# Optimization experiments

Hardware: AMD Instinct MI355X
Metric: run time of the kernel (lower is better)

The kernel has to match this reference:

```python
import jax, jax.numpy as jnp
import numpy as np

B, S, H = 32, 512, 2048
FP, SP = 1024, 1024


def setup_inputs() -> dict:
    key = jax.random.key(0)
    ks = jax.random.split(key, 8)
    X = jax.random.normal(ks[0], (B, S, H), dtype=jnp.float32)
    pY = jax.random.randint(ks[1], (B, S), 0, 3)
    # Y must be consistent with pY: hcw rows index [2, 2+FP), roo rows [2+FP, 2+FP+SP)
    y_hcw = jax.random.randint(ks[2], (B, S), 2, 2 + FP)
    y_roo = jax.random.randint(ks[3], (B, S), 2 + FP, 2 + FP + SP)
    Y = jnp.where(pY == 1, y_hcw, jnp.where(pY == 2, y_roo, 0))
    sc = 1.0 / np.sqrt(H)
    W_end = jax.random.normal(ks[4], (1, H), dtype=jnp.float32) * sc
    b_end = jnp.zeros((1,), jnp.float32)
    W_hcw = jax.random.normal(ks[5], (FP, H), dtype=jnp.float32) * sc
    b_hcw = jnp.zeros((FP,), jnp.float32)
    W_roo = jax.random.normal(ks[6], (SP, H), dtype=jnp.float32) * sc
    b_roo = jnp.zeros((SP,), jnp.float32)
    return {"X": X, "pY": pY, "Y": Y, "W_end": W_end, "b_end": b_end,
            "W_hcw": W_hcw, "b_hcw": b_hcw, "W_roo": W_roo, "b_roo": b_roo}


def reference(X, pY, Y, W_end, b_end, W_hcw, b_hcw, W_roo, b_roo):
    b, s, h = X.shape
    N = b * s
    Xf = X.reshape(N, h)
    pYf = pY.reshape(N)
    Yf = Y.reshape(N)

    end_mask = pYf == 0
    hcw_mask = pYf == 1
    roo_mask = pYf == 2

    # end head (Bernoulli prob)
    end_logit = Xf @ W_end.T + b_end            # [N, 1]
    end_prob = jax.nn.sigmoid(end_logit)[:, 0]  # [N]
    non_end = 1.0 - end_prob

    # hcw / roo heads: dense compute over all tokens, masked results match
    # the torch gather/scatter exactly at valid positions.
    P_hcw = jax.nn.softmax(Xf @ W_hcw.T + b_hcw, axis=-1)  # [N, FP]
    P_roo = jax.nn.softmax(Xf @ W_roo.T + b_roo, axis=-1)  # [N, SP]

    fp = W_hcw.shape[0]
    sp = W_roo.shape[0]
    idx_hcw = jnp.clip(Yf - 2, 0, fp - 1)
    idx_roo = jnp.clip(Yf - 2 - fp, 0, sp - 1)
    prob_hcw = jnp.take_along_axis(P_hcw, idx_hcw[:, None], axis=1)[:, 0]
    prob_roo = jnp.take_along_axis(P_roo, idx_roo[:, None], axis=1)[:, 0]

    prob = jnp.where(end_mask, end_prob,
                     jnp.where(hcw_mask, prob_hcw * non_end,
                               jnp.where(roo_mask, prob_roo * non_end, 1.0)))

    em = end_mask.astype(X.dtype)[:, None]
    hm = hcw_mask.astype(X.dtype)[:, None]
    rm = roo_mask.astype(X.dtype)[:, None]
    col_end = jnp.broadcast_to(end_prob[:, None], (N, 2)) * em        # [N, 2]
    col_hcw = P_hcw * non_end[:, None] * hm                           # [N, FP]
    col_roo = P_roo * non_end[:, None] * rm                           # [N, SP]
    prob_all_mat = jnp.concatenate([col_end, col_hcw, col_roo], axis=-1)

    log_prob = jnp.log(prob)
    return log_prob.reshape(b, s), prob_all_mat.reshape(b, s, fp + sp + 2)
```

## Files before the change

kernel.cpp:

```cpp
#include <hip/hip_runtime.h>
#include <hip/hip_bf16.h>
#include <cstddef>
#include <cstdint>

#define N_TOK 16384
#define H_    2048
#define FP_   1024
#define SP_   1024
#define C_    2050

#define BM 128
#define BN 128
#define BK 64
#define KP 72

typedef short bf16x8 __attribute__((ext_vector_type(8)));
typedef float f32x4  __attribute__((ext_vector_type(4)));

__device__ __forceinline__ unsigned pack_bf2(float a, float b) {
  __hip_bfloat16 x = __float2bfloat16(a);
  __hip_bfloat16 y = __float2bfloat16(b);
  unsigned short ux, uy;
  __builtin_memcpy(&ux, &x, 2);
  __builtin_memcpy(&uy, &y, 2);
  return (unsigned)ux | ((unsigned)uy << 16);
}

__device__ __forceinline__ unsigned short f2bf(float f) {
  __hip_bfloat16 h = __float2bfloat16(f);
  unsigned short u;
  __builtin_memcpy(&u, &h, 2);
  return u;
}

__device__ __forceinline__ float bf2f(unsigned short u) {
  unsigned v = (unsigned)u << 16;
  float f;
  __builtin_memcpy(&f, &v, 4);
  return f;
}

__global__ __launch_bounds__(256) void convert_kernel(
    const float* __restrict__ X,
    const float* __restrict__ W_hcw, const float* __restrict__ W_roo,
    const float* __restrict__ W_end, const float* __restrict__ b_end,
    unsigned short* __restrict__ Xb, unsigned short* __restrict__ Wb,
    float* __restrict__ mat)
{
  const int wave = threadIdx.x >> 6;
  const int lane = threadIdx.x & 63;
  const int row  = (blockIdx.x << 2) + wave;
  const bool isX = row < N_TOK;
  const float* src;
  unsigned short* dst;
  if (isX) {
    src = X + (size_t)row * H_;
    dst = Xb + (size_t)row * H_;
  } else {
    const int m = row - N_TOK;
    src = (m < FP_) ? (W_hcw + (size_t)m * H_) : (W_roo + (size_t)(m - FP_) * H_);
    dst = Wb + (size_t)m * H_;
  }
  float s = 0.f;
#pragma unroll
  for (int i = 0; i < 8; ++i) {
    const int e = (lane << 2) + (i << 8);
    float4 v = *(const float4*)(src + e);
    uint2 p;
    p.x = pack_bf2(v.x, v.y);
    p.y = pack_bf2(v.z, v.w);
    *(uint2*)(dst + e) = p;
    if (isX) {
      float4 w = *(const float4*)(W_end + e);
      s += v.x * w.x + v.y * w.y + v.z * w.z + v.w * w.w;
    }
  }
  if (isX) {
#pragma unroll
    for (int o = 32; o; o >>= 1) s += __shfl_xor(s, o);
    if (lane == 0) mat[(size_t)row * C_] = s + b_end[0];
  }
}

__global__ __launch_bounds__(512) void gemm_8phase_kernel(
    const unsigned short* __restrict__ Xb, const unsigned short* __restrict__ Wb,
    const float* __restrict__ b_hcw, const float* __restrict__ b_roo,
    float* __restrict__ mat)
{
  __shared__ __align__(16) unsigned short As[2][256 * 64];
  __shared__ __align__(16) unsigned short Bs[2][256 * 64];

  const int c0 = blockIdx.x * 256;
  const int n0 = blockIdx.y * 256;
  const float* bias = (c0 < FP_) ? (b_hcw + c0) : (b_roo + (c0 - FP_));

  const int t    = threadIdx.x;
  const int wave = t >> 6;
  const int lane = t & 63;
  const int wr   = wave >> 2;
  const int wc   = wave & 3;
  const int quad = lane >> 4;
  const int l16  = lane & 15;
  const int sw   = l16 & 7;

  const int srow = t >> 3;
  const int gch  = (t & 7) ^ (srow & 7);
  const unsigned short* gA = Xb + (size_t)(n0 + srow) * H_ + (gch << 3);
  const unsigned short* gB = Wb + (size_t)(c0 + srow) * H_ + (gch << 3);
  const int lds_off = srow * 64 + ((t & 7) << 3);

  auto stage = [&](int buf, int k0) {
#pragma unroll
    for (int r = 0; r < 4; ++r) {
      __builtin_amdgcn_global_load_lds(
          (const __attribute__((address_space(1))) unsigned int*)(gA + (size_t)(r * 64) * H_ + k0),
          (__attribute__((address_space(3))) unsigned int*)(&As[buf][r * 4096 + lds_off]),
          16, 0, 0);
      __builtin_amdgcn_global_load_lds(
          (const __attribute__((address_space(1))) unsigned int*)(gB + (size_t)(r * 64) * H_ + k0),
          (__attribute__((address_space(3))) unsigned int*)(&Bs[buf][r * 4096 + lds_off]),
          16, 0, 0);
    }
  };

  f32x4 acc[8][4];
#pragma unroll
  for (int i = 0; i < 8; ++i)
#pragma unroll
    for (int j = 0; j < 4; ++j)
#pragma unroll
      for (int r = 0; r < 4; ++r) acc[i][j][r] = 0.f;

  const int arow = wr * 128 + l16;
  const int brow = wc * 64 + l16;

  stage(0, 0);
  stage(1, 64);

  bf16x8 a[4][2], b[2][2];

#pragma unroll 1
  for (int tk = 0; tk < 32; ++tk) {
    const int cur = tk & 1;
    if (tk < 31) { asm volatile("s_waitcnt vmcnt(8)" ::: "memory"); }
    else         { asm volatile("s_waitcnt vmcnt(0)" ::: "memory"); }
    __builtin_amdgcn_sched_barrier(0);
    __builtin_amdgcn_s_barrier();

    const unsigned short* A_ = &As[cur][0];
    const unsigned short* B_ = &Bs[cur][0];

#pragma unroll
    for (int i = 0; i < 4; ++i)
#pragma unroll
      for (int kk = 0; kk < 2; ++kk)
        a[i][kk] = *(const bf16x8*)&A_[(arow + i * 16) * 64 + ((((kk << 2) + quad) ^ sw) << 3)];
#pragma unroll
    for (int j = 0; j < 2; ++j)
#pragma unroll
      for (int kk = 0; kk < 2; ++kk)
        b[j][kk] = *(const bf16x8*)&B_[(brow + j * 16) * 64 + ((((kk << 2) + quad) ^ sw) << 3)];
    __builtin_amdgcn_s_barrier();
    asm volatile("s_waitcnt lgkmcnt(0)" ::: "memory");
    __builtin_amdgcn_sched_barrier(0);
    __builtin_amdgcn_s_setprio(1);
#pragma unroll
    for (int i = 0; i < 4; ++i)
#pragma unroll
      for (int j = 0; j < 2; ++j)
#pragma unroll
        for (int kk = 0; kk < 2; ++kk)
          acc[i][j] = __builtin_amdgcn_mfma_f32_16x16x32_bf16(a[i][kk], b[j][kk], acc[i][j], 0, 0, 0);
    __builtin_amdgcn_s_setprio(0);
    __builtin_amdgcn_s_barrier();

#pragma unroll
    for (int j = 0; j < 2; ++j)
#pragma unroll
      for (int kk = 0; kk < 2; ++kk)
        b[j][kk] = *(const bf16x8*)&B_[(brow + (j + 2) * 16) * 64 + ((((kk << 2) + quad) ^ sw) << 3)];
    __builtin_amdgcn_s_barrier();
    asm volatile("s_waitcnt lgkmcnt(0)" ::: "memory");
    __builtin_amdgcn_sched_barrier(0);
    __builtin_amdgcn_s_setprio(1);
#pragma unroll
    for (int i = 0; i < 4; ++i)
#pragma unroll
      for (int j = 0; j < 2; ++j)
#pragma unroll
        for (int kk = 0; kk < 2; ++kk)
          acc[i][j + 2] = __builtin_amdgcn_mfma_f32_16x16x32_bf16(a[i][kk], b[j][kk], acc[i][j + 2], 0, 0, 0);
    __builtin_amdgcn_s_setprio(0);
    __builtin_amdgcn_s_barrier();

#pragma unroll
    for (int i = 0; i < 4; ++i)
#pragma unroll
      for (int kk = 0; kk < 2; ++kk)
        a[i][kk] = *(const bf16x8*)&A_[(arow + (i + 4) * 16) * 64 + ((((kk << 2) + quad) ^ sw) << 3)];
    __builtin_amdgcn_s_barrier();
    asm volatile("s_waitcnt lgkmcnt(0)" ::: "memory");
    __builtin_amdgcn_sched_barrier(0);
    __builtin_amdgcn_s_setprio(1);
#pragma unroll
    for (int i = 0; i < 4; ++i)
#pragma unroll
      for (int j = 0; j < 2; ++j)
#pragma unroll
        for (int kk = 0; kk < 2; ++kk)
          acc[i + 4][j + 2] = __builtin_amdgcn_mfma_f32_16x16x32_bf16(a[i][kk], b[j][kk], acc[i + 4][j + 2], 0, 0, 0);
    __builtin_amdgcn_s_setprio(0);
    __builtin_amdgcn_s_barrier();

#pragma unroll
    for (int j = 0; j < 2; ++j)
#pragma unroll
      for (int kk = 0; kk < 2; ++kk)
        b[j][kk] = *(const bf16x8*)&B_[(brow + j * 16) * 64 + ((((kk << 2) + quad) ^ sw) << 3)];
    __builtin_amdgcn_s_barrier();
    asm volatile("s_waitcnt lgkmcnt(0)" ::: "memory");
    __builtin_amdgcn_sched_barrier(0);
    __builtin_amdgcn_s_setprio(1);
#pragma unroll
    for (int i = 0; i < 4; ++i)
#pragma unroll
      for (int j = 0; j < 2; ++j)
#pragma unroll
        for (int kk = 0; kk < 2; ++kk)
          acc[i + 4][j] = __builtin_amdgcn_mfma_f32_16x16x32_bf16(a[i][kk], b[j][kk], acc[i + 4][j], 0, 0, 0);
    __builtin_amdgcn_s_setprio(0);
    __builtin_amdgcn_s_barrier();

    if (tk < 30) stage(cur, (tk + 2) << 6);
  }

  float bj[4];
#pragma unroll
  for (int j = 0; j < 4; ++j) bj[j] = bias[wc * 64 + j * 16 + l16];
#pragma unroll
  for (int i = 0; i < 8; ++i) {
#pragma unroll
    for (int r = 0; r < 4; ++r) {
      const int row = n0 + wr * 128 + i * 16 + quad * 4 + r;
      unsigned short* dst =
          (unsigned short*)(mat + (size_t)row * C_ + 4) + c0 + wc * 64 + l16;
#pragma unroll
      for (int j = 0; j < 4; ++j) dst[j * 16] = f2bf(acc[i][j][r] + bj[j]);
    }
  }
}

__global__ __launch_bounds__(256) void end_head_kernel(
    const float* __restrict__ X, const float* __restrict__ W_end,
    const float* __restrict__ b_end, float* __restrict__ mat)
{
  const int wave = threadIdx.x >> 6;
  const int lane = threadIdx.x & 63;
  const int n = (blockIdx.x << 2) + wave;
  const float* x = X + (size_t)n * H_;
  float s = 0.f;
#pragma unroll
  for (int i = 0; i < 8; ++i) {
    const int e = (lane + (i << 6)) << 2;
    float4 xv = *(const float4*)(x + e);
    float4 wv = *(const float4*)(W_end + e);
    s += xv.x * wv.x + xv.y * wv.y + xv.z * wv.z + xv.w * wv.w;
  }
#pragma unroll
  for (int o = 32; o; o >>= 1) s += __shfl_xor(s, o);
  if (lane == 0) mat[(size_t)n * C_] = s + b_end[0];
}

__global__ __launch_bounds__(256) void logits_gemm_fused(
    const float* __restrict__ X,
    const float* __restrict__ W_hcw, const float* __restrict__ W_roo,
    const float* __restrict__ b_hcw, const float* __restrict__ b_roo,
    float* __restrict__ mat)
{
  __shared__ __align__(16) unsigned short As[BM * KP];
  __shared__ __align__(16) unsigned short Bs[BN * KP];

  const int c0 = blockIdx.x * BN;
  const int n0 = blockIdx.y * BM;
  const float* Wbase = (c0 < FP_) ? (W_hcw + (size_t)c0 * H_)
                                  : (W_roo + (size_t)(c0 - FP_) * H_);
  const float* bias  = (c0 < FP_) ? (b_hcw + c0) : (b_roo + (c0 - FP_));

  const int t    = threadIdx.x;
  const int wave = t >> 6;
  const int lane = t & 63;
  const int wy   = wave >> 1;
  const int wx   = wave & 1;
  const int quad = lane >> 4;
  const int l16  = lane & 15;
  const int tq = t & 3;
  const int tr = t >> 2;

  f32x4 acc[4][4];
#pragma unroll
  for (int i = 0; i < 4; ++i)
#pragma unroll
    for (int j = 0; j < 4; ++j)
#pragma unroll
      for (int r = 0; r < 4; ++r) acc[i][j][r] = 0.f;

  for (int k0 = 0; k0 < H_; k0 += BK) {
#pragma unroll
    for (int p = 0; p < 2; ++p) {
      const int row = tr + (p << 6);
      const float4* xs = (const float4*)(X + (size_t)(n0 + row) * H_ + k0 + (tq << 4));
      const float4* ws = (const float4*)(Wbase + (size_t)row * H_ + k0 + (tq << 4));
      float4 x0 = xs[0], x1 = xs[1], x2 = xs[2], x3 = xs[3];
      float4 w0 = ws[0], w1 = ws[1], w2 = ws[2], w3 = ws[3];
      uint4 ua0 = {pack_bf2(x0.x, x0.y), pack_bf2(x0.z, x0.w),
                   pack_bf2(x1.x, x1.y), pack_bf2(x1.z, x1.w)};
      uint4 ua1 = {pack_bf2(x2.x, x2.y), pack_bf2(x2.z, x2.w),
                   pack_bf2(x3.x, x3.y), pack_bf2(x3.z, x3.w)};
      uint4 ub0 = {pack_bf2(w0.x, w0.y), pack_bf2(w0.z, w0.w),
                   pack_bf2(w1.x, w1.y), pack_bf2(w1.z, w1.w)};
      uint4 ub1 = {pack_bf2(w2.x, w2.y), pack_bf2(w2.z, w2.w),
                   pack_bf2(w3.x, w3.y), pack_bf2(w3.z, w3.w)};
      *(uint4*)&As[row * KP + (tq << 4)]     = ua0;
      *(uint4*)&As[row * KP + (tq << 4) + 8] = ua1;
      *(uint4*)&Bs[row * KP + (tq << 4)]     = ub0;
      *(uint4*)&Bs[row * KP + (tq << 4) + 8] = ub1;
    }
    __syncthreads();
#pragma unroll
    for (int kk = 0; kk < 2; ++kk) {
      bf16x8 af[4], bfr[4];
#pragma unroll
      for (int i = 0; i < 4; ++i)
        af[i] = *(const bf16x8*)&As[(wy * 64 + i * 16 + l16) * KP + kk * 32 + quad * 8];
#pragma unroll
      for (int j = 0; j < 4; ++j)
        bfr[j] = *(const bf16x8*)&Bs[(wx * 64 + j * 16 + l16) * KP + kk * 32 + quad * 8];
#pragma unroll
      for (int i = 0; i < 4; ++i)
#pragma unroll
        for (int j = 0; j < 4; ++j)
          acc[i][j] = __builtin_amdgcn_mfma_f32_16x16x32_bf16(af[i], bfr[j], acc[i][j], 0, 0, 0);
    }
    __syncthreads();
  }

  float bj[4];
#pragma unroll
  for (int j = 0; j < 4; ++j) bj[j] = bias[wx * 64 + j * 16 + l16];
#pragma unroll
  for (int i = 0; i < 4; ++i) {
#pragma unroll
    for (int r = 0; r < 4; ++r) {
      const int row = n0 + wy * 64 + i * 16 + quad * 4 + r;
      unsigned short* dst =
          (unsigned short*)(mat + (size_t)row * C_ + 4) + c0 + wx * 64 + l16;
#pragma unroll
      for (int j = 0; j < 4; ++j) dst[j * 16] = f2bf(acc[i][j][r] + bj[j]);
    }
  }
}

__global__ __launch_bounds__(256) void epilogue_kernel(
    const int* __restrict__ pY, const int* __restrict__ Yf,
    float* __restrict__ logp, float* __restrict__ mat)
{
  __shared__ float red[4];
  const int n = blockIdx.x;
  const int t = threadIdx.x;
  float* row = mat + (size_t)n * C_;
  const unsigned short* lg = (const unsigned short*)(row + 4);

  const int py = pY[n];
  const int y  = Yf[n];

  uint2 p0 = *(const uint2*)(lg + (t << 3));
  uint2 p1 = *(const uint2*)(lg + (t << 3) + 4);
  const float z = row[0];
  const int ih = min(max(y - 2, 0), FP_ - 1);
  const int ir = min(max(y - 2 - FP_, 0), SP_ - 1);
  const float lh = bf2f(lg[ih]);
  const float lr = bf2f(lg[FP_ + ir]);

  unsigned u[4] = {p0.x, p0.y, p1.x, p1.y};
  float e8[8];
  float s = 0.f;
#pragma unroll
  for (int i = 0; i < 4; ++i) {
    e8[2 * i]     = expf(bf2f((unsigned short)(u[i] & 0xffffu)));
    e8[2 * i + 1] = expf(bf2f((unsigned short)(u[i] >> 16)));
    s += e8[2 * i] + e8[2 * i + 1];
  }
#pragma unroll
  for (int o = 32; o; o >>= 1) s += __shfl_xor(s, o);
  const int w = t >> 6;
  if ((t & 63) == 0) red[w] = s;
  __syncthreads();
  const float Sh = red[0] + red[1];
  const float Sr = red[2] + red[3];

  const float sig = 1.f / (1.f + expf(-z));
  const float ne  = 1.f - sig;
  const float sc = (t < 128) ? ((py == 1) ? ne / Sh : 0.f)
                             : ((py == 2) ? ne / Sr : 0.f);
  float2* wp = (float2*)(row + 2 + (t << 3));
  wp[0] = make_float2(e8[0] * sc, e8[1] * sc);
  wp[1] = make_float2(e8[2] * sc, e8[3] * sc);
  wp[2] = make_float2(e8[4] * sc, e8[5] * sc);
  wp[3] = make_float2(e8[6] * sc, e8[7] * sc);
  if (t == 0) {
    const float ev = (py == 0) ? sig : 0.f;
    row[0] = ev;
    row[1] = ev;
    const float l1p   = log1pf(expf(-fabsf(z)));
    const float sp_z  = fmaxf(z, 0.f)  + l1p;
    const float sp_mz = fmaxf(-z, 0.f) + l1p;
    float lp;
    if      (py == 0) lp = -sp_mz;
    else if (py == 1) lp = (lh - logf(Sh)) - sp_z;
    else if (py == 2) lp = (lr - logf(Sr)) - sp_z;
    else              lp = 0.f;
    logp[n] = lp;
  }
}

extern "C" void kernel_launch(void* const* d_in, const int* in_sizes, int n_in,
                              void* d_out, int out_size, void* d_ws, size_t ws_size,
                              hipStream_t stream) {
  const float* X     = (const float*)d_in[0];
  const int*   pY    = (const int*)  d_in[1];
  const int*   Y     = (const int*)  d_in[2];
  const float* W_end = (const float*)d_in[3];
  const float* b_end = (const float*)d_in[4];
  const float* W_hcw = (const float*)d_in[5];
  const float* b_hcw = (const float*)d_in[6];
  const float* W_roo = (const float*)d_in[7];
  const float* b_roo = (const float*)d_in[8];

  float* out  = (float*)d_out;
  float* logp = out;
  float* mat  = out + N_TOK;

  const size_t xb_bytes = (size_t)N_TOK * H_ * 2;
  const size_t wb_bytes = (size_t)(FP_ + SP_) * H_ * 2;

  if (ws_size >= xb_bytes + wb_bytes) {
    unsigned short* Xb = (unsigned short*)d_ws;
    unsigned short* Wb = (unsigned short*)((char*)d_ws + xb_bytes);
    convert_kernel<<<(N_TOK + FP_ + SP_) / 4, 256, 0, stream>>>(
        X, W_hcw, W_roo, W_end, b_end, Xb, Wb, mat);
    dim3 g8(2048 / 256, N_TOK / 256);
    gemm_8phase_kernel<<<g8, 512, 0, stream>>>(Xb, Wb, b_hcw, b_roo, mat);
  } else {
    dim3 g(2048 / BN, N_TOK / BM);
    end_head_kernel<<<N_TOK / 4, 256, 0, stream>>>(X, W_end, b_end, mat);
    logits_gemm_fused<<<g, 256, 0, stream>>>(X, W_hcw, W_roo, b_hcw, b_roo, mat);
  }
  epilogue_kernel<<<N_TOK, 256, 0, stream>>>(pY, Y, logp, mat);
}
```

Baseline: 447.4 us.

## Split next-tile loads into half-tile stages interleaved across MFMA phases

The shared-memory tiles are reorganised into two halves that match the order in which the four MFMA phases consume A and B rows. The single bulk prefetch at the end of each k-iteration, which ran two tiles ahead, is replaced by a one-tile-ahead prefetch. Its loads are spread over the phases, issued right after the half of the other buffer they overwrite has been read. The aim is to smooth vector-memory issue and overlap it with matrix work. In exchange, the prefetch distance drops from two k-tiles to one, which leaves less slack to hide global load latency.

Measured after the change: 436.5 us. 2.4% less time.

```diff
diff --git a/kernel.cpp b/kernel.cpp
--- a/kernel.cpp
+++ b/kernel.cpp
@@ -87,8 +87,8 @@
     const float* __restrict__ b_hcw, const float* __restrict__ b_roo,
     float* __restrict__ mat)
 {
-  __shared__ __align__(16) unsigned short As[2][256 * 64];
-  __shared__ __align__(16) unsigned short Bs[2][256 * 64];
+  __shared__ __align__(16) unsigned short As[2][2 * 128 * 64];
+  __shared__ __align__(16) unsigned short Bs[2][2 * 128 * 64];
 
   const int c0 = blockIdx.x * 256;
   const int n0 = blockIdx.y * 256;
@@ -103,25 +103,29 @@
   const int l16  = lane & 15;
   const int sw   = l16 & 7;
 
-  const int srow = t >> 3;
-  const int gch  = (t & 7) ^ (srow & 7);
-  const unsigned short* gA = Xb + (size_t)(n0 + srow) * H_ + (gch << 3);
-  const unsigned short* gB = Wb + (size_t)(c0 + srow) * H_ + (gch << 3);
-  const int lds_off = srow * 64 + ((t & 7) << 3);
-
-  auto stage = [&](int buf, int k0) {
-#pragma unroll
-    for (int r = 0; r < 4; ++r) {
-      __builtin_amdgcn_global_load_lds(
-          (const __attribute__((address_space(1))) unsigned int*)(gA + (size_t)(r * 64) * H_ + k0),
-          (__attribute__((address_space(3))) unsigned int*)(&As[buf][r * 4096 + lds_off]),
-          16, 0, 0);
-      __builtin_amdgcn_global_load_lds(
-          (const __attribute__((address_space(1))) unsigned int*)(gB + (size_t)(r * 64) * H_ + k0),
-          (__attribute__((address_space(3))) unsigned int*)(&Bs[buf][r * 4096 + lds_off]),
-          16, 0, 0);
-    }
+  const int tA   = t >> 3;
+  const int gofs = (((t & 7) ^ (tA & 7)) << 3);
+  const int ldst = tA * 64 + ((t & 7) << 3);
+  const unsigned short* gA0 = Xb + (size_t)n0 * H_ + gofs;
+  const unsigned short* gB0 = Wb + (size_t)c0 * H_ + gofs;
+  const int growB = ((tA >> 5) << 6) + (tA & 31);
+
+  auto stageA = [&](int buf, int h, int s, int k0) {
+    __builtin_amdgcn_global_load_lds(
+        (const __attribute__((address_space(1))) unsigned int*)
+            (gA0 + (size_t)(s * 128 + h * 64 + tA) * H_ + k0),
+        (__attribute__((address_space(3))) unsigned int*)
+            (&As[buf][h * 8192 + s * 4096 + ldst]),
+        16, 0, 0);
   };
+  auto stageB = [&](int buf, int h, int s, int k0) {
+    __builtin_amdgcn_global_load_lds(
+        (const __attribute__((address_space(1))) unsigned int*)
+            (gB0 + (size_t)(s * 128 + h * 32 + growB) * H_ + k0),
+        (__attribute__((address_space(3))) unsigned int*)
+            (&Bs[buf][h * 8192 + s * 4096 + ldst]),
+        16, 0, 0);
+  };
 
   f32x4 acc[8][4];
 #pragma unroll
@@ -131,19 +135,29 @@
 #pragma unroll
       for (int r = 0; r < 4; ++r) acc[i][j][r] = 0.f;
 
-  const int arow = wr * 128 + l16;
-  const int brow = wc * 64 + l16;
-
-  stage(0, 0);
-  stage(1, 64);
+  const int aprow = wr * 64 + l16;
+  const int bprow = wc * 32 + l16;
+
+  stageA(0, 0, 0, 0); stageA(0, 0, 1, 0);
+  stageB(0, 0, 0, 0); stageB(0, 0, 1, 0);
+  stageB(0, 1, 0, 0); stageB(0, 1, 1, 0);
+  stageA(0, 1, 0, 0); stageA(0, 1, 1, 0);
 
   bf16x8 a[4][2], b[2][2];
 
 #pragma unroll 1
   for (int tk = 0; tk < 32; ++tk) {
     const int cur = tk & 1;
-    if (tk < 31) { asm volatile("s_waitcnt vmcnt(8)" ::: "memory"); }
-    else         { asm volatile("s_waitcnt vmcnt(0)" ::: "memory"); }
+    const int oth = cur ^ 1;
+    const int kN  = (tk + 1) << 6;
+
+    if (tk < 31) {
+      stageA(oth, 0, 0, kN); stageA(oth, 0, 1, kN);
+      stageB(oth, 0, 0, kN); stageB(oth, 0, 1, kN);
+      asm volatile("s_waitcnt vmcnt(4)" ::: "memory");
+    } else {
+      asm volatile("s_waitcnt vmcnt(0)" ::: "memory");
+    }
     __builtin_amdgcn_sched_barrier(0);
     __builtin_amdgcn_s_barrier();
 
@@ -154,12 +168,13 @@
     for (int i = 0; i < 4; ++i)
 #pragma unroll
       for (int kk = 0; kk < 2; ++kk)
-        a[i][kk] = *(const bf16x8*)&A_[(arow + i * 16) * 64 + ((((kk << 2) + quad) ^ sw) << 3)];
+        a[i][kk] = *(const bf16x8*)&A_[(aprow + i * 16) * 64 + ((((kk << 2) + quad) ^ sw) << 3)];
 #pragma unroll
     for (int j = 0; j < 2; ++j)
 #pragma unroll
       for (int kk = 0; kk < 2; ++kk)
-        b[j][kk] = *(const bf16x8*)&B_[(brow + j * 16) * 64 + ((((kk << 2) + quad) ^ sw) << 3)];
+        b[j][kk] = *(const bf16x8*)&B_[(bprow + j * 16) * 64 + ((((kk << 2) + quad) ^ sw) << 3)];
+    if (tk < 31) { stageB(oth, 1, 0, kN); stageB(oth, 1, 1, kN); }
     __builtin_amdgcn_s_barrier();
     asm volatile("s_waitcnt lgkmcnt(0)" ::: "memory");
     __builtin_amdgcn_sched_barrier(0);
@@ -178,7 +193,8 @@
     for (int j = 0; j < 2; ++j)
 #pragma unroll
       for (int kk = 0; kk < 2; ++kk)
-        b[j][kk] = *(const bf16x8*)&B_[(brow + (j + 2) * 16) * 64 + ((((kk << 2) + quad) ^ sw) << 3)];
+        b[j][kk] = *(const bf16x8*)&B_[8192 + (bprow + j * 16) * 64 + ((((kk << 2) + quad) ^ sw) << 3)];
+    if (tk < 31) { stageA(oth, 1, 0, kN); stageA(oth, 1, 1, kN); }
     __builtin_amdgcn_s_barrier();
     asm volatile("s_waitcnt lgkmcnt(0)" ::: "memory");
     __builtin_amdgcn_sched_barrier(0);
@@ -197,7 +213,7 @@
     for (int i = 0; i < 4; ++i)
 #pragma unroll
       for (int kk = 0; kk < 2; ++kk)
-        a[i][kk] = *(const bf16x8*)&A_[(arow + (i + 4) * 16) * 64 + ((((kk << 2) + quad) ^ sw) << 3)];
+        a[i][kk] = *(const bf16x8*)&A_[8192 + (aprow + i * 16) * 64 + ((((kk << 2) + quad) ^ sw) << 3)];
     __builtin_amdgcn_s_barrier();
     asm volatile("s_waitcnt lgkmcnt(0)" ::: "memory");
     __builtin_amdgcn_sched_barrier(0);
@@ -216,7 +232,7 @@
     for (int j = 0; j < 2; ++j)
 #pragma unroll
       for (int kk = 0; kk < 2; ++kk)
-        b[j][kk] = *(const bf16x8*)&B_[(brow + j * 16) * 64 + ((((kk << 2) + quad) ^ sw) << 3)];
+        b[j][kk] = *(const bf16x8*)&B_[(bprow + j * 16) * 64 + ((((kk << 2) + quad) ^ sw) << 3)];
     __builtin_amdgcn_s_barrier();
     asm volatile("s_waitcnt lgkmcnt(0)" ::: "memory");
     __builtin_amdgcn_sched_barrier(0);
@@ -230,8 +246,6 @@
           acc[i + 4][j] = __builtin_amdgcn_mfma_f32_16x16x32_bf16(a[i][kk], b[j][kk], acc[i + 4][j], 0, 0, 0);
     __builtin_amdgcn_s_setprio(0);
     __builtin_amdgcn_s_barrier();
-
-    if (tk < 30) stage(cur, (tk + 2) << 6);
   }
 
   float bj[4];
```
